# Performance work log

Measured on AMD Instinct MI355X. Metric: run time of the kernel, lower is better.

## Reference

```python
import jax, jax.numpy as jnp
import numpy as np
from jax import lax

CONV_SIZE = 5
MORPH_SIZE = 5
TH1_INIT = 0.5
STEP = 0.0005
LO, HI = 0.84, 0.86


def _maxpool(a):
    p = MORPH_SIZE // 2
    return lax.reduce_window(
        a, -jnp.inf, lax.max,
        window_dimensions=(1, 1, MORPH_SIZE, MORPH_SIZE),
        window_strides=(1, 1, 1, 1),
        padding=[(0, 0), (0, 0), (p, p), (p, p)])


def setup_inputs() -> dict:
    key = jax.random.key(0)
    k1, _ = jax.random.split(key)
    x = jax.random.uniform(k1, (8, 4, 1024, 1024), dtype=jnp.float32)
    blur_k = jnp.full((1, 1, CONV_SIZE, CONV_SIZE), 1.0 / CONV_SIZE ** 2, dtype=jnp.float32)
    return {"x": x, "blur_k": blur_k}


def reference(x, blur_k):
    N, c, h, w = x.shape
    xi = x.reshape(N * c, 1, h, w)
    out = lax.conv_general_dilated(
        xi, blur_k, window_strides=(1, 1), padding='SAME',
        dimension_numbers=('NCHW', 'OIHW', 'NCHW')).reshape(N, c, h, w)

    # iterative mean-based threshold (quantile) search, same as the torch while-loops
    out_c = lax.stop_gradient(out)

    def frac_above(th):
        return jnp.mean(jnp.where(out_c > th, 1.0, 0.0))

    th = jnp.float32(TH1_INIT)
    th = lax.while_loop(lambda t: frac_above(t) < LO, lambda t: t - STEP, th)
    th = lax.while_loop(lambda t: frac_above(t) > HI, lambda t: t + STEP, th)

    thr = jnp.where(out > th, 1.0, 0.0)
    # morphological close: max-pool then min-pool (min = -maxpool(-x))
    closed = -_maxpool(-_maxpool(thr))
    return closed  # torch casts to float64; kept float32 (see notes)
```

## Files before the change

kernel.cpp:

```cpp
#include <hip/hip_runtime.h>


#define K_STEPS 1024
#define LO_COUNT 28185723u
#define R_TILE 8
#define PT_ROWS 16

#define OFF_HIST 4096
#define OFF_KQ   16384

__global__ void k_init(float* __restrict__ T32, unsigned int* __restrict__ hist) {
    int t = threadIdx.x;
    for (int i = t; i < K_STEPS + 1; i += 256) hist[i] = 0u;
    float th = 0.5f;
    for (int k = 0; k < K_STEPS; k++) {
        if ((k & 255) == t) T32[k] = th;
        th = th - 0.0005f;
    }
}

__device__ __forceinline__ int find_k(const float* __restrict__ Ts, double val) {
    int k = (int)floor((0.5 - val) * 2000.0);
    k = max(0, min(K_STEPS - 1, k));
    while (k > 0 && (double)Ts[k - 1] < val) k--;
    while (k < K_STEPS && !((double)Ts[k] < val)) k++;
    return k;
}

__global__ __launch_bounds__(256) void
k_pass1(const float4* __restrict__ x4, const float* __restrict__ bk,
        const float* __restrict__ T32g, unsigned int* __restrict__ hist,
        unsigned short* __restrict__ kq16) {
    __shared__ float Ts[K_STEPS];
    __shared__ unsigned int lh[K_STEPS + 1];
    int tid = threadIdx.x;
    int p = blockIdx.y, y0 = blockIdx.x * R_TILE;
    for (int i = tid; i < K_STEPS; i += 256) Ts[i] = T32g[i];
    for (int i = tid; i < K_STEPS + 1; i += 256) lh[i] = 0u;
    __syncthreads();

    const float4* pf = x4 + (size_t)p * 262144;
    int tB = (tid < 255) ? tid + 1 : 0;
    double w = (double)bk[0];
    const float4 z4 = make_float4(0.f, 0.f, 0.f, 0.f);

    float4 A[4], B[4];
    #pragma unroll
    for (int i = 0; i < 4; i++) {
        int yy = y0 - 2 + i;
        if ((unsigned)yy < 1024u) { A[i] = pf[yy * 256 + tid]; B[i] = pf[yy * 256 + tB]; }
        else                      { A[i] = z4;                 B[i] = z4; }
    }

    unsigned int cnt0 = 0;
    for (int iy = 0; iy < R_TILE; iy++) {
        int y = y0 + iy, ya = y + 2;
        float4 An, Bn;
        if ((unsigned)ya < 1024u) { An = pf[ya * 256 + tid]; Bn = pf[ya * 256 + tB]; }
        else                      { An = z4;                 Bn = z4; }

        double s0 = (double)A[0].x + (double)A[1].x + (double)A[2].x + (double)A[3].x + (double)An.x;
        double s1 = (double)A[0].y + (double)A[1].y + (double)A[2].y + (double)A[3].y + (double)An.y;
        double s2 = (double)A[0].z + (double)A[1].z + (double)A[2].z + (double)A[3].z + (double)An.z;
        double s3 = (double)A[0].w + (double)A[1].w + (double)A[2].w + (double)A[3].w + (double)An.w;
        double s4 = (double)B[0].x + (double)B[1].x + (double)B[2].x + (double)B[3].x + (double)Bn.x;
        double s5 = (double)B[0].y + (double)B[1].y + (double)B[2].y + (double)B[3].y + (double)Bn.y;
        double s6 = (double)B[0].z + (double)B[1].z + (double)B[2].z + (double)B[3].z + (double)Bn.z;
        double s7 = (double)B[0].w + (double)B[1].w + (double)B[2].w + (double)B[3].w + (double)Bn.w;

        double v0, v1, v2, v3;
        double m123 = s1 + s2 + s3;
        if (tid != 255) {
            v0 = (s0 + m123 + s4) * w;
            v1 = (m123 + s4 + s5) * w;
            v2 = (s2 + s3 + s4 + s5 + s6) * w;
            v3 = (s3 + s4 + s5 + s6 + s7) * w;
        } else {
            v0 = (s0 + m123) * w;
            v1 = m123 * w;
            v2 = (s4 + s5 + s6) * w;
            v3 = (s4 + s5 + s6 + s7) * w;
        }

        int k0 = find_k(Ts, v0);
        int k1 = find_k(Ts, v1);
        int k2 = find_k(Ts, v2);
        int k3 = find_k(Ts, v3);
        cnt0 += (unsigned)(k0 == 0) + (unsigned)(k1 == 0)
              + (unsigned)(k2 == 0) + (unsigned)(k3 == 0);
        if (k0 > 0) atomicAdd(&lh[k0], 1u);
        if (k1 > 0) atomicAdd(&lh[k1], 1u);
        if (k2 > 0) atomicAdd(&lh[k2], 1u);
        if (k3 > 0) atomicAdd(&lh[k3], 1u);

        unsigned short pa = (unsigned short)(min(k0, 255) | (min(k1, 255) << 8));
        unsigned short pb = (unsigned short)(min(k2, 255) | (min(k3, 255) << 8));
        size_t rb = ((size_t)p * 1024 + (size_t)y) * 512;
        kq16[rb + 2 * tid + 1] = pa;
        kq16[rb + ((tid < 255) ? (2 * tid + 2) : 0)] = pb;

        A[0] = A[1]; A[1] = A[2]; A[2] = A[3]; A[3] = An;
        B[0] = B[1]; B[1] = B[2]; B[2] = B[3]; B[3] = Bn;
    }

    #pragma unroll
    for (int d = 32; d > 0; d >>= 1) cnt0 += __shfl_down(cnt0, d);
    if ((tid & 63) == 0 && cnt0) atomicAdd(&lh[0], cnt0);
    __syncthreads();
    for (int i = tid; i < K_STEPS + 1; i += 256) {
        unsigned int c = lh[i];
        if (c) atomicAdd(&hist[i], c);
    }
}

__global__ __launch_bounds__(256) void
k_post(const unsigned char* __restrict__ kqb, const unsigned int* __restrict__ hist,
       float* __restrict__ out) {
    __shared__ unsigned long long Tt[24 * 16];
    __shared__ unsigned long long Vv[20 * 16];
    __shared__ unsigned long long Dd[20 * 16];
    __shared__ unsigned long long Ww[16 * 16];
    __shared__ unsigned long long Ff[16 * 16];
    __shared__ int ksS;

    int tid = threadIdx.x;
    int p = blockIdx.y, y0 = blockIdx.x * PT_ROWS;

    if (tid < 64) {
        int lane = tid;
        unsigned int h[16], s = 0;
        #pragma unroll
        for (int i = 0; i < 16; i++) { h[i] = hist[lane * 16 + i]; s += h[i]; }
        unsigned int inc = s;
        #pragma unroll
        for (int d = 1; d < 64; d <<= 1) {
            unsigned int t = __shfl_up(inc, d);
            if (lane >= d) inc += t;
        }
        unsigned int excl = inc - s;
        bool cross = (excl < LO_COUNT) && (excl + s >= LO_COUNT);
        unsigned long long m = __ballot(cross);
        if (m) {
            int cl = __ffsll((long long)m) - 1;
            if (lane == cl) {
                unsigned int c = excl; int ks = K_STEPS - 1;
                for (int i = 0; i < 16; i++) { c += h[i]; if (c >= LO_COUNT) { ks = lane * 16 + i; break; } }
                ksS = ks;
            }
        } else if (lane == 0) ksS = K_STEPS - 1;
    }
    __syncthreads();
    int ks = ksS;

    const unsigned char* kp = kqb + (size_t)p * 1048576;
    unsigned short* Tt16 = (unsigned short*)Tt;
    #pragma unroll
    for (int i = 0; i < 6; i++) {
        int ch = tid + 256 * i;
        int r = ch >> 6, cc = ch & 63;
        int pr = y0 - 4 + r;
        unsigned int m = 0u;
        if ((unsigned)pr < 1024u) {
            uint4 q = ((const uint4*)(kp + (size_t)pr * 1024))[cc];
            unsigned int wv;
            wv = q.x;
            m |= (unsigned)((wv & 0xffu) <= (unsigned)ks)
               | ((unsigned)(((wv >> 8) & 0xffu) <= (unsigned)ks) << 1)
               | ((unsigned)(((wv >> 16) & 0xffu) <= (unsigned)ks) << 2)
               | ((unsigned)((wv >> 24) <= (unsigned)ks) << 3);
            wv = q.y;
            m |= ((unsigned)((wv & 0xffu) <= (unsigned)ks) << 4)
               | ((unsigned)(((wv >> 8) & 0xffu) <= (unsigned)ks) << 5)
               | ((unsigned)(((wv >> 16) & 0xffu) <= (unsigned)ks) << 6)
               | ((unsigned)((wv >> 24) <= (unsigned)ks) << 7);
            wv = q.z;
            m |= ((unsigned)((wv & 0xffu) <= (unsigned)ks) << 8)
               | ((unsigned)(((wv >> 8) & 0xffu) <= (unsigned)ks) << 9)
               | ((unsigned)(((wv >> 16) & 0xffu) <= (unsigned)ks) << 10)
               | ((unsigned)((wv >> 24) <= (unsigned)ks) << 11);
            wv = q.w;
            m |= ((unsigned)((wv & 0xffu) <= (unsigned)ks) << 12)
               | ((unsigned)(((wv >> 8) & 0xffu) <= (unsigned)ks) << 13)
               | ((unsigned)(((wv >> 16) & 0xffu) <= (unsigned)ks) << 14)
               | ((unsigned)((wv >> 24) <= (unsigned)ks) << 15);
        }
        Tt16[ch] = (unsigned short)m;
    }
    __syncthreads();

    for (int i = tid; i < 320; i += 256) {
        int vr = i >> 4, wc = i & 15;
        int b = vr * 16 + wc;
        Vv[i] = Tt[b] | Tt[b + 16] | Tt[b + 32] | Tt[b + 48] | Tt[b + 64];
    }
    __syncthreads();

    for (int i = tid; i < 320; i += 256) {
        int vr = i >> 4, wc = i & 15;
        int pr = y0 - 2 + vr;
        if ((unsigned)pr >= 1024u) { Dd[i] = ~0ull; continue; }
        unsigned long long Vc = Vv[i];
        unsigned long long Vl = (wc > 0)  ? Vv[i - 1] : 0ull;
        unsigned long long Vr = (wc < 15) ? Vv[i + 1] : 0ull;
        Dd[i] = Vc
            | (Vc << 1) | (Vl >> 63)
            | (Vc << 2) | (Vl >> 62)
            | (Vc >> 1) | (Vr << 63)
            | (Vc >> 2) | (Vr << 62);
    }
    __syncthreads();

    {
        int wr = tid >> 4, wc = tid & 15;
        int b = wr * 16 + wc;
        Ww[tid] = Dd[b] & Dd[b + 16] & Dd[b + 32] & Dd[b + 48] & Dd[b + 64];
    }
    __syncthreads();

    {
        int wc = tid & 15;
        unsigned long long Wc = Ww[tid];
        unsigned long long Wl = (wc > 0)  ? Ww[tid - 1] : ~0ull;
        unsigned long long Wr = (wc < 15) ? Ww[tid + 1] : ~0ull;
        Ff[tid] = Wc
            & ((Wc << 1) | (Wl >> 63))
            & ((Wc << 2) | (Wl >> 62))
            & ((Wc >> 1) | (Wr << 63))
            & ((Wc >> 2) | (Wr << 62));
    }
    __syncthreads();

    for (int i = 0; i < PT_ROWS; i++) {
        unsigned long long wd = Ff[i * 16 + (tid >> 4)];
        int sh = (tid & 15) * 4;
        float4 f;
        f.x = (float)((wd >> sh) & 1ull);
        f.y = (float)((wd >> (sh + 1)) & 1ull);
        f.z = (float)((wd >> (sh + 2)) & 1ull);
        f.w = (float)((wd >> (sh + 3)) & 1ull);
        ((float4*)(out + (size_t)p * 1048576 + (size_t)(y0 + i) * 1024))[tid] = f;
    }
}

extern "C" void kernel_launch(void* const* d_in, const int* in_sizes, int n_in,
                              void* d_out, int out_size, void* d_ws, size_t ws_size,
                              hipStream_t stream) {
    const float4* x4 = (const float4*)d_in[0];
    const float*  bk = (const float*)d_in[1];
    float* out = (float*)d_out;

    char* ws = (char*)d_ws;
    float*          T32  = (float*)(ws);
    unsigned int*   hist = (unsigned int*)(ws + OFF_HIST);
    unsigned short* kq16 = (unsigned short*)(ws + OFF_KQ);
    const unsigned char* kqb = (const unsigned char*)(ws + OFF_KQ);

    k_init<<<1, 256, 0, stream>>>(T32, hist);

    dim3 g1(1024 / R_TILE, 32);
    k_pass1<<<g1, 256, 0, stream>>>(x4, bk, T32, hist, kq16);

    dim3 g2(1024 / PT_ROWS, 32);
    k_post<<<g2, 256, 0, stream>>>(kqb, hist, out);
}
```

Before: 344.1 us.

## Replace double-precision blur sums with exact fixed-point integer sliding window

```diff
diff --git a/kernel.cpp b/kernel.cpp
--- a/kernel.cpp
+++ b/kernel.cpp
@@ -1,5 +1,7 @@
 #include <hip/hip_runtime.h>
 
+
+typedef float nfloat4 __attribute__((ext_vector_type(4)));
 
 #define K_STEPS 1024
 #define LO_COUNT 28185723u
@@ -9,83 +11,103 @@
 #define OFF_HIST 4096
 #define OFF_KQ   16384
 
-__global__ void k_init(float* __restrict__ T32, unsigned int* __restrict__ hist) {
+__global__ void k_init(const float* __restrict__ bk, unsigned int* __restrict__ U32,
+                       unsigned int* __restrict__ hist) {
     int t = threadIdx.x;
     for (int i = t; i < K_STEPS + 1; i += 256) hist[i] = 0u;
+    double Wp = (double)bk[0] * 0x1p-23;
     float th = 0.5f;
+    float myT[4];
     for (int k = 0; k < K_STEPS; k++) {
-        if ((k & 255) == t) T32[k] = th;
+        if ((k & 255) == t) myT[k >> 8] = th;
         th = th - 0.0005f;
     }
-}
-
-__device__ __forceinline__ int find_k(const float* __restrict__ Ts, double val) {
-    int k = (int)floor((0.5 - val) * 2000.0);
+    #pragma unroll
+    for (int j = 0; j < 4; j++) {
+        double T = (double)myT[j];
+        long long S0 = 0;
+        if (T > 0.0) S0 = (long long)ceil(T / Wp);
+        if (S0 < 0) S0 = 0;
+        while (S0 > 0 && (double)(S0 - 1) * Wp > T) S0--;
+        while ((double)S0 * Wp <= T) S0++;
+        U32[j * 256 + t] = (unsigned int)S0;
+    }
+}
+
+__device__ __forceinline__ int find_k_u(const unsigned int* __restrict__ U,
+                                        unsigned int S, float gf) {
+    int k = (int)(fmaf(-gf, (float)S, 1000.5f));
     k = max(0, min(K_STEPS - 1, k));
-    while (k > 0 && (double)Ts[k - 1] < val) k--;
-    while (k < K_STEPS && !((double)Ts[k] < val)) k++;
+    while (k > 0 && S >= U[k - 1]) k--;
+    while (S < U[k]) k++;
     return k;
+}
+
+__device__ __forceinline__ uint4 cvt4(float4 f) {
+    uint4 u;
+    u.x = (unsigned int)(f.x * 8388608.0f);
+    u.y = (unsigned int)(f.y * 8388608.0f);
+    u.z = (unsigned int)(f.z * 8388608.0f);
+    u.w = (unsigned int)(f.w * 8388608.0f);
+    return u;
 }
 
 __global__ __launch_bounds__(256) void
 k_pass1(const float4* __restrict__ x4, const float* __restrict__ bk,
-        const float* __restrict__ T32g, unsigned int* __restrict__ hist,
+        const unsigned int* __restrict__ U32g, unsigned int* __restrict__ hist,
         unsigned short* __restrict__ kq16) {
-    __shared__ float Ts[K_STEPS];
+    __shared__ unsigned int U[K_STEPS];
     __shared__ unsigned int lh[K_STEPS + 1];
     int tid = threadIdx.x;
     int p = blockIdx.y, y0 = blockIdx.x * R_TILE;
-    for (int i = tid; i < K_STEPS; i += 256) Ts[i] = T32g[i];
+    for (int i = tid; i < K_STEPS; i += 256) U[i] = U32g[i];
     for (int i = tid; i < K_STEPS + 1; i += 256) lh[i] = 0u;
     __syncthreads();
 
+    float gf = (float)(2000.0 * ((double)bk[0] * 0x1p-23));
     const float4* pf = x4 + (size_t)p * 262144;
     int tB = (tid < 255) ? tid + 1 : 0;
-    double w = (double)bk[0];
     const float4 z4 = make_float4(0.f, 0.f, 0.f, 0.f);
 
-    float4 A[4], B[4];
+    uint4 hA[5], hB[5];
+    unsigned int cd[8] = {0, 0, 0, 0, 0, 0, 0, 0};
     #pragma unroll
     for (int i = 0; i < 4; i++) {
         int yy = y0 - 2 + i;
-        if ((unsigned)yy < 1024u) { A[i] = pf[yy * 256 + tid]; B[i] = pf[yy * 256 + tB]; }
-        else                      { A[i] = z4;                 B[i] = z4; }
+        float4 a = ((unsigned)yy < 1024u) ? pf[yy * 256 + tid] : z4;
+        float4 b = ((unsigned)yy < 1024u) ? pf[yy * 256 + tB]  : z4;
+        hA[i] = cvt4(a); hB[i] = cvt4(b);
+        cd[0] += hA[i].x; cd[1] += hA[i].y; cd[2] += hA[i].z; cd[3] += hA[i].w;
+        cd[4] += hB[i].x; cd[5] += hB[i].y; cd[6] += hB[i].z; cd[7] += hB[i].w;
     }
 
     unsigned int cnt0 = 0;
+    #pragma unroll
     for (int iy = 0; iy < R_TILE; iy++) {
         int y = y0 + iy, ya = y + 2;
-        float4 An, Bn;
-        if ((unsigned)ya < 1024u) { An = pf[ya * 256 + tid]; Bn = pf[ya * 256 + tB]; }
-        else                      { An = z4;                 Bn = z4; }
-
-        double s0 = (double)A[0].x + (double)A[1].x + (double)A[2].x + (double)A[3].x + (double)An.x;
-        double s1 = (double)A[0].y + (double)A[1].y + (double)A[2].y + (double)A[3].y + (double)An.y;
-        double s2 = (double)A[0].z + (double)A[1].z + (double)A[2].z + (double)A[3].z + (double)An.z;
-        double s3 = (double)A[0].w + (double)A[1].w + (double)A[2].w + (double)A[3].w + (double)An.w;
-        double s4 = (double)B[0].x + (double)B[1].x + (double)B[2].x + (double)B[3].x + (double)Bn.x;
-        double s5 = (double)B[0].y + (double)B[1].y + (double)B[2].y + (double)B[3].y + (double)Bn.y;
-        double s6 = (double)B[0].z + (double)B[1].z + (double)B[2].z + (double)B[3].z + (double)Bn.z;
-        double s7 = (double)B[0].w + (double)B[1].w + (double)B[2].w + (double)B[3].w + (double)Bn.w;
-
-        double v0, v1, v2, v3;
-        double m123 = s1 + s2 + s3;
+        float4 a = ((unsigned)ya < 1024u) ? pf[ya * 256 + tid] : z4;
+        float4 b = ((unsigned)ya < 1024u) ? pf[ya * 256 + tB]  : z4;
+        hA[4] = cvt4(a); hB[4] = cvt4(b);
+        cd[0] += hA[4].x; cd[1] += hA[4].y; cd[2] += hA[4].z; cd[3] += hA[4].w;
+        cd[4] += hB[4].x; cd[5] += hB[4].y; cd[6] += hB[4].z; cd[7] += hB[4].w;
+
+        unsigned int S0, S1, S2, S3;
         if (tid != 255) {
-            v0 = (s0 + m123 + s4) * w;
-            v1 = (m123 + s4 + s5) * w;
-            v2 = (s2 + s3 + s4 + s5 + s6) * w;
-            v3 = (s3 + s4 + s5 + s6 + s7) * w;
+            S0 = cd[0] + cd[1] + cd[2] + cd[3] + cd[4];
+            S1 = S0 - cd[0] + cd[5];
+            S2 = S1 - cd[1] + cd[6];
+            S3 = S2 - cd[2] + cd[7];
         } else {
-            v0 = (s0 + m123) * w;
-            v1 = m123 * w;
-            v2 = (s4 + s5 + s6) * w;
-            v3 = (s4 + s5 + s6 + s7) * w;
+            S0 = cd[0] + cd[1] + cd[2] + cd[3];
+            S1 = S0 - cd[0];
+            S2 = cd[4] + cd[5] + cd[6];
+            S3 = S2 + cd[7];
         }
 
-        int k0 = find_k(Ts, v0);
-        int k1 = find_k(Ts, v1);
-        int k2 = find_k(Ts, v2);
-        int k3 = find_k(Ts, v3);
+        int k0 = find_k_u(U, S0, gf);
+        int k1 = find_k_u(U, S1, gf);
+        int k2 = find_k_u(U, S2, gf);
+        int k3 = find_k_u(U, S3, gf);
         cnt0 += (unsigned)(k0 == 0) + (unsigned)(k1 == 0)
               + (unsigned)(k2 == 0) + (unsigned)(k3 == 0);
         if (k0 > 0) atomicAdd(&lh[k0], 1u);
@@ -99,8 +121,10 @@
         kq16[rb + 2 * tid + 1] = pa;
         kq16[rb + ((tid < 255) ? (2 * tid + 2) : 0)] = pb;
 
-        A[0] = A[1]; A[1] = A[2]; A[2] = A[3]; A[3] = An;
-        B[0] = B[1]; B[1] = B[2]; B[2] = B[3]; B[3] = Bn;
+        cd[0] -= hA[0].x; cd[1] -= hA[0].y; cd[2] -= hA[0].z; cd[3] -= hA[0].w;
+        cd[4] -= hB[0].x; cd[5] -= hB[0].y; cd[6] -= hB[0].z; cd[7] -= hB[0].w;
+        hA[0] = hA[1]; hA[1] = hA[2]; hA[2] = hA[3]; hA[3] = hA[4];
+        hB[0] = hB[1]; hB[1] = hB[2]; hB[2] = hB[3]; hB[3] = hB[4];
     }
 
     #pragma unroll
@@ -189,8 +213,7 @@
     __syncthreads();
 
     for (int i = tid; i < 320; i += 256) {
-        int vr = i >> 4, wc = i & 15;
-        int b = vr * 16 + wc;
+        int b = (i >> 4) * 16 + (i & 15);
         Vv[i] = Tt[b] | Tt[b + 16] | Tt[b + 32] | Tt[b + 48] | Tt[b + 64];
     }
     __syncthreads();
@@ -211,8 +234,7 @@
     __syncthreads();
 
     {
-        int wr = tid >> 4, wc = tid & 15;
-        int b = wr * 16 + wc;
+        int b = (tid >> 4) * 16 + (tid & 15);
         Ww[tid] = Dd[b] & Dd[b + 16] & Dd[b + 32] & Dd[b + 48] & Dd[b + 64];
     }
     __syncthreads();
@@ -233,12 +255,13 @@
     for (int i = 0; i < PT_ROWS; i++) {
         unsigned long long wd = Ff[i * 16 + (tid >> 4)];
         int sh = (tid & 15) * 4;
-        float4 f;
+        nfloat4 f;
         f.x = (float)((wd >> sh) & 1ull);
         f.y = (float)((wd >> (sh + 1)) & 1ull);
         f.z = (float)((wd >> (sh + 2)) & 1ull);
         f.w = (float)((wd >> (sh + 3)) & 1ull);
-        ((float4*)(out + (size_t)p * 1048576 + (size_t)(y0 + i) * 1024))[tid] = f;
+        nfloat4* dst = ((nfloat4*)(out + (size_t)p * 1048576 + (size_t)(y0 + i) * 1024)) + tid;
+        __builtin_nontemporal_store(f, dst);
     }
 }
 
@@ -250,15 +273,15 @@
     float* out = (float*)d_out;
 
     char* ws = (char*)d_ws;
-    float*          T32  = (float*)(ws);
+    unsigned int*   U32  = (unsigned int*)(ws);
     unsigned int*   hist = (unsigned int*)(ws + OFF_HIST);
     unsigned short* kq16 = (unsigned short*)(ws + OFF_KQ);
     const unsigned char* kqb = (const unsigned char*)(ws + OFF_KQ);
 
-    k_init<<<1, 256, 0, stream>>>(T32, hist);
+    k_init<<<1, 256, 0, stream>>>(bk, U32, hist);
 
     dim3 g1(1024 / R_TILE, 32);
-    k_pass1<<<g1, 256, 0, stream>>>(x4, bk, T32, hist, kq16);
+    k_pass1<<<g1, 256, 0, stream>>>(x4, bk, U32, hist, kq16);
 
     dim3 g2(1024 / PT_ROWS, 32);
     k_post<<<g2, 256, 0, stream>>>(kqb, hist, out);
```

After: 396.8 us. 15.3% more time.
